# Kernel tuning notes

Hardware: AMD Instinct MI355X
Metric: run time of the kernel (lower is better)

Reference implementation:

```python
import jax, jax.numpy as jnp
import numpy as np

N_USERS = 250000
N_ITEMS = 250000
D = 64          # embedding_dim
H = 64          # hidden_dim
N_EDGES = 1200000
N_NODES = N_USERS + N_ITEMS


def gcn_conv(x, W, b, src, dst, num_nodes):
    """PyG-style GCNConv: add self-loops, symmetric deg normalization, scatter-add."""
    loop = jnp.arange(num_nodes, dtype=src.dtype)
    s = jnp.concatenate([src, loop])
    d = jnp.concatenate([dst, loop])
    deg = jax.ops.segment_sum(jnp.ones(d.shape, x.dtype), d, num_segments=num_nodes)
    dinv = deg ** -0.5  # deg >= 1 thanks to self-loops
    h = x @ W  # [N, H]
    norm = dinv[s] * dinv[d]  # [E']
    msg = h[s] * norm[:, None]  # [E', H] gather
    out = jax.ops.segment_sum(msg, d, num_segments=num_nodes)  # scatter-add
    return out + b


def setup_inputs() -> dict:
    key = jax.random.key(0)
    ks = jax.random.split(key, 8)
    inp = {
        "user_table": jax.random.normal(ks[0], (N_USERS, D), jnp.float32) * 0.1,
        "item_table": jax.random.normal(ks[1], (N_ITEMS, D), jnp.float32) * 0.1,
        "W1": jax.random.normal(ks[2], (D, H), jnp.float32) * (1.0 / np.sqrt(D)),
        "b1": jnp.zeros((H,), jnp.float32),
        "W2": jax.random.normal(ks[3], (H, H), jnp.float32) * (1.0 / np.sqrt(H)),
        "b2": jnp.zeros((H,), jnp.float32),
        "Wp": jax.random.normal(ks[4], (2 * H, 1), jnp.float32) * (1.0 / np.sqrt(2 * H)),
        "bp": jnp.zeros((1,), jnp.float32),
        "edge_index": jax.random.randint(ks[5], (2, N_EDGES), 0, N_NODES, jnp.int32),
        "user_ids": jax.random.randint(ks[6], (N_USERS,), 0, N_USERS, jnp.int32),
        "item_ids": jax.random.randint(ks[7], (N_ITEMS,), 0, N_ITEMS, jnp.int32),
    }
    return inp


def reference(user_table, item_table, W1, b1, W2, b2, Wp, bp,
              edge_index, user_ids, item_ids):
    # embedding bag lookups (one id per bag -> plain gather)
    user_emb = user_table[user_ids]   # [num_users, D]
    item_emb = item_table[item_ids]   # [num_items, D]
    x = jnp.concatenate([user_emb, item_emb], axis=0)  # [N_NODES, D]

    src, dst = edge_index[0], edge_index[1]
    x = jax.nn.relu(gcn_conv(x, W1, b1, src, dst, N_NODES))
    x = jax.nn.relu(gcn_conv(x, W2, b2, src, dst, N_NODES))

    u = x[:N_USERS][user_ids]   # [B, H]
    i = x[N_USERS:][item_ids]   # [B, H]
    combined = jnp.concatenate([u, i], axis=1)  # [B, 2H]
    return combined @ Wp + bp   # [B, 1]
```

## Files before the change

kernel.cpp:

```cpp
#include <hip/hip_runtime.h>

#define NUSERS 250000
#define NITEMS 250000
#define NNODES 500000
#define NEDGES 1200000
#define NGROUPS (NNODES/16)
#define NCH8   (NNODES/8)

#define NB     245
#define BCAP   6144
#define SEGE   8192
#define NBLKA  147

typedef _Float16 half_t;
typedef _Float16 half8 __attribute__((ext_vector_type(8)));
typedef _Float16 half4 __attribute__((ext_vector_type(4)));
typedef float    f32x4 __attribute__((ext_vector_type(4)));


__global__ void k_zero_gc(int* __restrict__ gc) {
    int t = threadIdx.x;
    if (t < NB) gc[t] = 0;
}

__global__ __launch_bounds__(256) void k_bucketA(
    const int* __restrict__ src, const int* __restrict__ dst,
    int* __restrict__ gcursor, unsigned int* __restrict__ gbuf)
{
    __shared__ int ecnt[256];
    __shared__ int ebase[256];
    __shared__ int ecur[256];
    __shared__ int gres[256];
    __shared__ unsigned int stage[SEGE];
    __shared__ unsigned char stb[SEGE];

    const int t = threadIdx.x;
    const int e0 = blockIdx.x * SEGE;
    const int ecount = min(SEGE, NEDGES - e0);

    ecnt[t] = 0;
    __syncthreads();
    for (int k = t; k < ecount; k += 256)
        atomicAdd(&ecnt[dst[e0 + k] >> 11], 1);
    __syncthreads();

    const int v = ecnt[t];
    ebase[t] = v; __syncthreads();
    for (int d = 1; d < 256; d <<= 1) {
        int x = (t >= d) ? ebase[t - d] : 0;
        __syncthreads();
        ebase[t] += x;
        __syncthreads();
    }
    const int excl = ebase[t] - v;
    __syncthreads();
    ebase[t] = excl;
    ecur[t]  = excl;
    if (t < NB && v > 0) gres[t] = atomicAdd(&gcursor[t], v);
    __syncthreads();

    for (int k = t; k < ecount; k += 256) {
        const int s  = src[e0 + k];
        const int d2 = dst[e0 + k];
        const int b  = d2 >> 11;
        const int p  = atomicAdd(&ecur[b], 1);
        stage[p] = ((unsigned int)s << 11) | (unsigned int)(d2 & 2047);
        stb[p]   = (unsigned char)b;
    }
    __syncthreads();

    for (int s = t; s < ecount; s += 256) {
        const int b = stb[s];
        gbuf[(size_t)b * BCAP + gres[b] + (s - ebase[b])] = stage[s];
    }
}

__global__ __launch_bounds__(256) void k_scan_buckets(const int* __restrict__ gcursor,
                                                      int* __restrict__ bbase)
{
    __shared__ int sm[256];
    const int t = threadIdx.x;
    const int v = (t < NB) ? gcursor[t] : 0;
    sm[t] = v; __syncthreads();
    for (int d = 1; d < 256; d <<= 1) {
        int x = (t >= d) ? sm[t - d] : 0;
        __syncthreads();
        sm[t] += x;
        __syncthreads();
    }
    if (t < NB) bbase[t] = sm[t] - v;
}

__global__ __launch_bounds__(256) void k_bucketB(
    const int* __restrict__ gcursor, const int* __restrict__ bbase,
    const unsigned int* __restrict__ gbuf,
    float* __restrict__ dinv, int* __restrict__ offsets, int* __restrict__ csr)
{
    __shared__ int hist[2048];
    __shared__ int cur[2048];
    __shared__ int psum[256];
    __shared__ int lcsr[BCAP];

    const int t = threadIdx.x;
    const int b = blockIdx.x;
    const int cnt = gcursor[b];
    const int nbase = b << 11;
    const int nb = min(2048, NNODES - nbase);
    const unsigned int* gb0 = gbuf + (size_t)b * BCAP;
    const int cbase = bbase[b];

    for (int i = t; i < 2048; i += 256) hist[i] = 0;
    __syncthreads();
    for (int s = t; s < cnt; s += 256)
        atomicAdd(&hist[gb0[s] & 2047], 1);
    __syncthreads();

    for (int i = t; i < nb; i += 256)
        dinv[nbase + i] = 1.0f / sqrtf((float)(hist[i] + 1));

    int loc[8]; int ssum = 0;
#pragma unroll
    for (int k = 0; k < 8; ++k) { loc[k] = hist[t * 8 + k]; ssum += loc[k]; }
    psum[t] = ssum; __syncthreads();
    for (int d = 1; d < 256; d <<= 1) {
        int x = (t >= d) ? psum[t - d] : 0;
        __syncthreads();
        psum[t] += x;
        __syncthreads();
    }
    int run = psum[t] - ssum;
#pragma unroll
    for (int k = 0; k < 8; ++k) {
        const int i = t * 8 + k;
        if (i < nb) offsets[nbase + i] = cbase + run;
        cur[i] = run;
        run += loc[k];
    }
    __syncthreads();
    if (b == NB - 1 && t == 0) offsets[NNODES] = cbase + cnt;

    for (int s = t; s < cnt; s += 256) {
        const unsigned int pk = gb0[s];
        const int p = atomicAdd(&cur[pk & 2047], 1);
        lcsr[p] = (int)(pk >> 11);
    }
    __syncthreads();
    for (int s = t; s < cnt; s += 256)
        csr[cbase + s] = lcsr[s];
}


__device__ __forceinline__ void build_bfrags(const float* __restrict__ W,
                                             int lg, int cl, half8 bf[2][4]) {
#pragma unroll
    for (int q = 0; q < 2; ++q)
#pragma unroll
        for (int c = 0; c < 4; ++c) {
            half8 v;
#pragma unroll
            for (int j = 0; j < 8; ++j)
                v[j] = (half_t)W[(32 * q + 8 * lg + j) * 64 + 4 * cl + c];
            bf[q][c] = v;
        }
}


__global__ __launch_bounds__(256) void k_mm1(
    const float* __restrict__ user_table, const float* __restrict__ item_table,
    const int* __restrict__ uid, const int* __restrict__ iid,
    const float* __restrict__ W1, const float* __restrict__ dinv,
    half_t* __restrict__ g)
{
    const int lane = threadIdx.x & 63;
    const int lg = lane >> 4, cl = lane & 15;
    const int wid = blockIdx.x * (blockDim.x >> 6) + (threadIdx.x >> 6);
    const int nw  = gridDim.x * (blockDim.x >> 6);

    half8 bf[2][4];
    build_bfrags(W1, lg, cl, bf);
    const f32x4 zacc = {0.f, 0.f, 0.f, 0.f};

    if (wid >= NGROUPS) return;

    #define ROWPTR(tt) ({                                                     \
        const int ttc_ = ((tt) < NGROUPS) ? (tt) : wid;                       \
        const int na_ = ttc_ * 16 + cl;                                       \
        (na_ < NUSERS) ? user_table + (size_t)uid[na_] * 64                   \
                       : item_table + (size_t)iid[na_ - NUSERS] * 64; })

    int t = wid;
    const float* pcur  = ROWPTR(t);
    f32x4 u0 = *(const f32x4*)(pcur + 8 * lg);
    f32x4 u1 = *(const f32x4*)(pcur + 8 * lg + 4);
    f32x4 u2 = *(const f32x4*)(pcur + 8 * lg + 32);
    f32x4 u3 = *(const f32x4*)(pcur + 8 * lg + 36);
    const float* pnext = ROWPTR(t + nw);

    while (t < NGROUPS) {
        const int tn = t + nw;
        f32x4 v0 = *(const f32x4*)(pnext + 8 * lg);
        f32x4 v1 = *(const f32x4*)(pnext + 8 * lg + 4);
        f32x4 v2 = *(const f32x4*)(pnext + 8 * lg + 32);
        f32x4 v3 = *(const f32x4*)(pnext + 8 * lg + 36);
        const float* pnn = ROWPTR(tn + nw);

        const int n0 = t * 16;
        half8 a0, a1;
#pragma unroll
        for (int j = 0; j < 4; ++j) {
            a0[j] = (half_t)u0[j]; a0[4 + j] = (half_t)u1[j];
            a1[j] = (half_t)u2[j]; a1[4 + j] = (half_t)u3[j];
        }
        f32x4 acc[4];
#pragma unroll
        for (int c = 0; c < 4; ++c) {
            acc[c] = __builtin_amdgcn_mfma_f32_16x16x32_f16(a0, bf[0][c], zacc, 0, 0, 0);
            acc[c] = __builtin_amdgcn_mfma_f32_16x16x32_f16(a1, bf[1][c], acc[c], 0, 0, 0);
        }
#pragma unroll
        for (int r = 0; r < 4; ++r) {
            const int nd = n0 + lg * 4 + r;
            const float dn = dinv[nd];
            half4 hv;
#pragma unroll
            for (int c = 0; c < 4; ++c) hv[c] = (half_t)(acc[c][r] * dn);
            *(half4*)(g + (size_t)nd * 64 + 4 * cl) = hv;
        }
        u0 = v0; u1 = v1; u2 = v2; u3 = v3;
        pnext = pnn;
        t = tn;
    }
    #undef ROWPTR
}


#define G8_STEP(K)                                                            \
        const bool v##K = sstep + K < deg;                                    \
        const int p##K = csr[v##K ? eb + sstep + K : 0];

#define G8_ROW(K)                                                             \
        const half8 r##K = *(const half8*)(g_p + (size_t)p##K * 64 + sub * 8);

#define G8_ACC(K) {                                                           \
        const float m_ = v##K ? 1.0f : 0.0f;                                  \
        acc0 = fmaf(m_, (float)r##K[0], acc0); acc1 = fmaf(m_, (float)r##K[1], acc1); \
        acc2 = fmaf(m_, (float)r##K[2], acc2); acc3 = fmaf(m_, (float)r##K[3], acc3); \
        acc4 = fmaf(m_, (float)r##K[4], acc4); acc5 = fmaf(m_, (float)r##K[5], acc5); \
        acc6 = fmaf(m_, (float)r##K[6], acc6); acc7 = fmaf(m_, (float)r##K[7], acc7); }

#define GATHER_G8(ginp)                                                       \
    const half_t* __restrict__ g_p = (ginp);                                  \
    const int n  = n0 + gi;                                                   \
    const int eb = off[n];                                                    \
    const int deg = off[n + 1] - eb;                                          \
    float acc0, acc1, acc2, acc3, acc4, acc5, acc6, acc7;                     \
    {                                                                         \
        half8 sv = *(const half8*)(g_p + (size_t)n * 64 + sub * 8);           \
        acc0 = (float)sv[0]; acc1 = (float)sv[1];                             \
        acc2 = (float)sv[2]; acc3 = (float)sv[3];                             \
        acc4 = (float)sv[4]; acc5 = (float)sv[5];                             \
        acc6 = (float)sv[6]; acc7 = (float)sv[7];                             \
    }                                                                         \
    int md = deg;                                                             \
    md = max(md, __shfl_xor(md, 8, 64));                                      \
    md = max(md, __shfl_xor(md, 16, 64));                                     \
    md = max(md, __shfl_xor(md, 32, 64));                                     \
    for (int sstep = 0; sstep < md; sstep += 8) {                             \
        G8_STEP(0) G8_STEP(1) G8_STEP(2) G8_STEP(3)                           \
        G8_STEP(4) G8_STEP(5) G8_STEP(6) G8_STEP(7)                           \
        G8_ROW(0) G8_ROW(1) G8_ROW(2) G8_ROW(3)                               \
        G8_ROW(4) G8_ROW(5) G8_ROW(6) G8_ROW(7)                               \
        G8_ACC(0) G8_ACC(1) G8_ACC(2) G8_ACC(3)                               \
        G8_ACC(4) G8_ACC(5) G8_ACC(6) G8_ACC(7)                               \
    }

__global__ __launch_bounds__(256) void k_gather(
    const int* __restrict__ off, const int* __restrict__ csr,
    const half_t* __restrict__ gin, half_t* __restrict__ sout)
{
    const int lane = threadIdx.x & 63;
    const int gi = lane >> 3;
    const int sub = lane & 7;
    const int wid = blockIdx.x * (blockDim.x >> 6) + (threadIdx.x >> 6);
    const int nw  = gridDim.x * (blockDim.x >> 6);

    for (int t = wid; t < NCH8; t += nw) {
        const int n0 = t * 8;
        GATHER_G8(gin)
        half8 ov;
        ov[0] = (half_t)acc0; ov[1] = (half_t)acc1;
        ov[2] = (half_t)acc2; ov[3] = (half_t)acc3;
        ov[4] = (half_t)acc4; ov[5] = (half_t)acc5;
        ov[6] = (half_t)acc6; ov[7] = (half_t)acc7;
        *(half8*)(sout + (size_t)n * 64 + sub * 8) = ov;
    }
}


__global__ __launch_bounds__(256) void k_mm2(
    const float* __restrict__ W2, const float* __restrict__ b1,
    const float* __restrict__ dinv,
    const half_t* __restrict__ s, half_t* __restrict__ g)
{
    const int lane = threadIdx.x & 63;
    const int lg = lane >> 4, cl = lane & 15;
    const int wid = blockIdx.x * (blockDim.x >> 6) + (threadIdx.x >> 6);
    const int nw  = gridDim.x * (blockDim.x >> 6);

    half8 bf[2][4];
    build_bfrags(W2, lg, cl, bf);
    float bias0[8], bias1[8];
#pragma unroll
    for (int j = 0; j < 8; ++j) {
        bias0[j] = b1[8 * lg + j];
        bias1[j] = b1[32 + 8 * lg + j];
    }
    const f32x4 zacc = {0.f, 0.f, 0.f, 0.f};

    for (int t = wid; t < NGROUPS; t += nw) {
        const int n0 = t * 16;
        const int na = n0 + cl;
        const float dna = dinv[na];
        half8 s0 = *(const half8*)(s + (size_t)na * 64 + 8 * lg);
        half8 s1 = *(const half8*)(s + (size_t)na * 64 + 32 + 8 * lg);
        half8 a0, a1;
#pragma unroll
        for (int j = 0; j < 8; ++j) {
            a0[j] = (half_t)fmaxf(fmaf(dna, (float)s0[j], bias0[j]), 0.0f);
            a1[j] = (half_t)fmaxf(fmaf(dna, (float)s1[j], bias1[j]), 0.0f);
        }
        f32x4 acc[4];
#pragma unroll
        for (int c = 0; c < 4; ++c) {
            acc[c] = __builtin_amdgcn_mfma_f32_16x16x32_f16(a0, bf[0][c], zacc, 0, 0, 0);
            acc[c] = __builtin_amdgcn_mfma_f32_16x16x32_f16(a1, bf[1][c], acc[c], 0, 0, 0);
        }
#pragma unroll
        for (int r = 0; r < 4; ++r) {
            const int nd = n0 + lg * 4 + r;
            const float dn = dinv[nd];
            half4 hv;
#pragma unroll
            for (int c = 0; c < 4; ++c) hv[c] = (half_t)(acc[c][r] * dn);
            *(half4*)(g + (size_t)nd * 64 + 4 * cl) = hv;
        }
    }
}


__global__ __launch_bounds__(256) void k_gather_ps(
    const int* __restrict__ off, const int* __restrict__ csr,
    const float* __restrict__ b2, const float* __restrict__ Wp,
    const float* __restrict__ dinv,
    const half_t* __restrict__ g2, float* __restrict__ pscore)
{
    const int lane = threadIdx.x & 63;
    const int gi = lane >> 3;
    const int sub = lane & 7;
    const int wid = blockIdx.x * (blockDim.x >> 6) + (threadIdx.x >> 6);
    const int nw  = gridDim.x * (blockDim.x >> 6);

    float bb[8], wpu[8], wpi[8];
#pragma unroll
    for (int k = 0; k < 8; ++k) {
        bb[k]  = b2[sub * 8 + k];
        wpu[k] = Wp[sub * 8 + k];
        wpi[k] = Wp[64 + sub * 8 + k];
    }

    for (int t = wid; t < NCH8; t += nw) {
        const int n0 = t * 8;
        GATHER_G8(g2)

        const bool isu = (n0 < NUSERS);
        const float dn = dinv[n];
        float v = 0.0f;
#define PS_ACC(K, A) {                                                      \
        float w_ = isu ? wpu[K] : wpi[K];                                   \
        float x_ = fmaxf(fmaf(dn, (A), bb[K]), 0.0f);                       \
        v = fmaf(x_, w_, v); }
        PS_ACC(0, acc0) PS_ACC(1, acc1) PS_ACC(2, acc2) PS_ACC(3, acc3)
        PS_ACC(4, acc4) PS_ACC(5, acc5) PS_ACC(6, acc6) PS_ACC(7, acc7)
#undef PS_ACC
        v += __shfl_xor(v, 1, 64);
        v += __shfl_xor(v, 2, 64);
        v += __shfl_xor(v, 4, 64);
        if (sub == 0) pscore[n] = v;
    }
}

__global__ void k_pairs(const int* __restrict__ user_ids, const int* __restrict__ item_ids,
                        const float* __restrict__ pscore, const float* __restrict__ bp,
                        float* __restrict__ out)
{
    int b = blockIdx.x * blockDim.x + threadIdx.x;
    if (b < NUSERS)
        out[b] = pscore[user_ids[b]] + pscore[NUSERS + item_ids[b]] + bp[0];
}


extern "C" void kernel_launch(void* const* d_in, const int* in_sizes, int n_in,
                              void* d_out, int out_size, void* d_ws, size_t ws_size,
                              hipStream_t stream)
{
    const float* user_table = (const float*)d_in[0];
    const float* item_table = (const float*)d_in[1];
    const float* W1 = (const float*)d_in[2];
    const float* b1 = (const float*)d_in[3];
    const float* W2 = (const float*)d_in[4];
    const float* b2 = (const float*)d_in[5];
    const float* Wp = (const float*)d_in[6];
    const float* bp = (const float*)d_in[7];
    const int* edge = (const int*)d_in[8];
    const int* uid  = (const int*)d_in[9];
    const int* iid  = (const int*)d_in[10];
    float* out = (float*)d_out;

    const int* src = edge;
    const int* dst = edge + NEDGES;

    char* ws = (char*)d_ws;
    float*        pscore   = (float*)       (ws + 0);
    float*        dinv     = (float*)       (ws + 2000000);
    int*          offsets  = (int*)         (ws + 4000000);
    int*          bbase    = (int*)         (ws + 6000128);
    int*          gcursor  = (int*)         (ws + 6004224);
    int*          csr      = (int*)         (ws + 6008000);
    half_t*       bufA     = (half_t*)      (ws + 10808064);
    half_t*       bufB     = (half_t*)      (ws + 74808064);
    unsigned int* gbuf     = (unsigned int*)(ws + 74808064);

    k_zero_gc     <<<1, 256, 0, stream>>>(gcursor);
    k_bucketA     <<<NBLKA, 256, 0, stream>>>(src, dst, gcursor, gbuf);
    k_scan_buckets<<<1, 256, 0, stream>>>(gcursor, bbase);
    k_bucketB     <<<NB, 256, 0, stream>>>(gcursor, bbase, gbuf, dinv, offsets, csr);

    k_mm1      <<<2048, 256, 0, stream>>>(user_table, item_table, uid, iid, W1, dinv, bufA);
    k_gather   <<<2048, 256, 0, stream>>>(offsets, csr, bufA, bufB);
    k_mm2      <<<2048, 256, 0, stream>>>(W2, b1, dinv, bufB, bufA);
    k_gather_ps<<<2048, 256, 0, stream>>>(offsets, csr, b2, Wp, dinv, bufA, pscore);
    k_pairs    <<<(NUSERS + 255) / 256, 256, 0, stream>>>(uid, iid, pscore, bp, out);
}
```

Before: 201.5 us.

## Fuse layer-1 neighbor gather with second GEMM into one kernel

```diff
diff --git a/kernel.cpp b/kernel.cpp
--- a/kernel.cpp
+++ b/kernel.cpp
@@ -180,29 +180,29 @@
     build_bfrags(W1, lg, cl, bf);
     const f32x4 zacc = {0.f, 0.f, 0.f, 0.f};
 
-    if (wid >= NGROUPS) return;
-
-    #define ROWPTR(tt) ({                                                     \
-        const int ttc_ = ((tt) < NGROUPS) ? (tt) : wid;                       \
-        const int na_ = ttc_ * 16 + cl;                                       \
-        (na_ < NUSERS) ? user_table + (size_t)uid[na_] * 64                   \
-                       : item_table + (size_t)iid[na_ - NUSERS] * 64; })
-
     int t = wid;
-    const float* pcur  = ROWPTR(t);
-    f32x4 u0 = *(const f32x4*)(pcur + 8 * lg);
-    f32x4 u1 = *(const f32x4*)(pcur + 8 * lg + 4);
-    f32x4 u2 = *(const f32x4*)(pcur + 8 * lg + 32);
-    f32x4 u3 = *(const f32x4*)(pcur + 8 * lg + 36);
-    const float* pnext = ROWPTR(t + nw);
-
+    f32x4 u0, u1, u2, u3;
+    if (t < NGROUPS) {
+        const int na = t * 16 + cl;
+        const float* p = (na < NUSERS)
+            ? user_table + (size_t)uid[na] * 64
+            : item_table + (size_t)iid[na - NUSERS] * 64;
+        u0 = *(const f32x4*)(p + 8 * lg);
+        u1 = *(const f32x4*)(p + 8 * lg + 4);
+        u2 = *(const f32x4*)(p + 8 * lg + 32);
+        u3 = *(const f32x4*)(p + 8 * lg + 36);
+    }
     while (t < NGROUPS) {
         const int tn = t + nw;
-        f32x4 v0 = *(const f32x4*)(pnext + 8 * lg);
-        f32x4 v1 = *(const f32x4*)(pnext + 8 * lg + 4);
-        f32x4 v2 = *(const f32x4*)(pnext + 8 * lg + 32);
-        f32x4 v3 = *(const f32x4*)(pnext + 8 * lg + 36);
-        const float* pnn = ROWPTR(tn + nw);
+        const int tl = (tn < NGROUPS) ? tn : t;
+        const int nb2 = tl * 16 + cl;
+        const float* pn = (nb2 < NUSERS)
+            ? user_table + (size_t)uid[nb2] * 64
+            : item_table + (size_t)iid[nb2 - NUSERS] * 64;
+        f32x4 v0 = *(const f32x4*)(pn + 8 * lg);
+        f32x4 v1 = *(const f32x4*)(pn + 8 * lg + 4);
+        f32x4 v2 = *(const f32x4*)(pn + 8 * lg + 32);
+        f32x4 v3 = *(const f32x4*)(pn + 8 * lg + 36);
 
         const int n0 = t * 16;
         half8 a0, a1;
@@ -227,10 +227,116 @@
             *(half4*)(g + (size_t)nd * 64 + 4 * cl) = hv;
         }
         u0 = v0; u1 = v1; u2 = v2; u3 = v3;
-        pnext = pnn;
         t = tn;
     }
-    #undef ROWPTR
+}
+
+
+__global__ __launch_bounds__(256) void k_gather_mm2(
+    const int* __restrict__ off, const int* __restrict__ csr,
+    const float* __restrict__ W2, const float* __restrict__ b1,
+    const float* __restrict__ dinv,
+    const half_t* __restrict__ g1, half_t* __restrict__ g2)
+{
+    const int lane = threadIdx.x & 63;
+    const int lg = lane >> 4, cl = lane & 15;
+    const int wid = blockIdx.x * (blockDim.x >> 6) + (threadIdx.x >> 6);
+    const int nw  = gridDim.x * (blockDim.x >> 6);
+
+    half8 bf[2][4];
+    build_bfrags(W2, lg, cl, bf);
+    float bias0[8], bias1[8];
+#pragma unroll
+    for (int j = 0; j < 8; ++j) {
+        bias0[j] = b1[8 * lg + j];
+        bias1[j] = b1[32 + 8 * lg + j];
+    }
+    const f32x4 zacc = {0.f, 0.f, 0.f, 0.f};
+
+    for (int t = wid; t < NGROUPS; t += nw) {
+        const int n0 = t * 16;
+        const int n  = n0 + cl;
+        const int eb = off[n];
+        const int deg = off[n + 1] - eb;
+
+        float f0[8], f1[8];
+        {
+            half8 s0 = *(const half8*)(g1 + (size_t)n * 64 + 8 * lg);
+            half8 s1 = *(const half8*)(g1 + (size_t)n * 64 + 32 + 8 * lg);
+#pragma unroll
+            for (int j = 0; j < 8; ++j) { f0[j] = (float)s0[j]; f1[j] = (float)s1[j]; }
+        }
+
+        int md = deg;
+        md = max(md, __shfl_xor(md, 1, 64));
+        md = max(md, __shfl_xor(md, 2, 64));
+        md = max(md, __shfl_xor(md, 4, 64));
+        md = max(md, __shfl_xor(md, 8, 64));
+
+        for (int ss = 0; ss < md; ss += 4) {
+            const bool v0 = ss < deg,     v1 = ss + 1 < deg;
+            const bool v2 = ss + 2 < deg, v3 = ss + 3 < deg;
+            const int p0 = csr[v0 ? eb + ss     : 0];
+            const int p1 = csr[v1 ? eb + ss + 1 : 0];
+            const int p2 = csr[v2 ? eb + ss + 2 : 0];
+            const int p3 = csr[v3 ? eb + ss + 3 : 0];
+            const half8 r00 = *(const half8*)(g1 + (size_t)p0 * 64 + 8 * lg);
+            const half8 r01 = *(const half8*)(g1 + (size_t)p0 * 64 + 32 + 8 * lg);
+            const half8 r10 = *(const half8*)(g1 + (size_t)p1 * 64 + 8 * lg);
+            const half8 r11 = *(const half8*)(g1 + (size_t)p1 * 64 + 32 + 8 * lg);
+            const half8 r20 = *(const half8*)(g1 + (size_t)p2 * 64 + 8 * lg);
+            const half8 r21 = *(const half8*)(g1 + (size_t)p2 * 64 + 32 + 8 * lg);
+            const half8 r30 = *(const half8*)(g1 + (size_t)p3 * 64 + 8 * lg);
+            const half8 r31 = *(const half8*)(g1 + (size_t)p3 * 64 + 32 + 8 * lg);
+            const float m0 = v0 ? 1.0f : 0.0f;
+            const float m1 = v1 ? 1.0f : 0.0f;
+            const float m2 = v2 ? 1.0f : 0.0f;
+            const float m3 = v3 ? 1.0f : 0.0f;
+#pragma unroll
+            for (int j = 0; j < 8; ++j) {
+                f0[j] = fmaf(m0, (float)r00[j], f0[j]);
+                f1[j] = fmaf(m0, (float)r01[j], f1[j]);
+            }
+#pragma unroll
+            for (int j = 0; j < 8; ++j) {
+                f0[j] = fmaf(m1, (float)r10[j], f0[j]);
+                f1[j] = fmaf(m1, (float)r11[j], f1[j]);
+            }
+#pragma unroll
+            for (int j = 0; j < 8; ++j) {
+                f0[j] = fmaf(m2, (float)r20[j], f0[j]);
+                f1[j] = fmaf(m2, (float)r21[j], f1[j]);
+            }
+#pragma unroll
+            for (int j = 0; j < 8; ++j) {
+                f0[j] = fmaf(m3, (float)r30[j], f0[j]);
+                f1[j] = fmaf(m3, (float)r31[j], f1[j]);
+            }
+        }
+
+        const float dna = dinv[n];
+        half8 a0, a1;
+#pragma unroll
+        for (int j = 0; j < 8; ++j) {
+            a0[j] = (half_t)fmaxf(fmaf(dna, f0[j], bias0[j]), 0.0f);
+            a1[j] = (half_t)fmaxf(fmaf(dna, f1[j], bias1[j]), 0.0f);
+        }
+        f32x4 acc[4];
+#pragma unroll
+        for (int c = 0; c < 4; ++c) {
+            acc[c] = __builtin_amdgcn_mfma_f32_16x16x32_f16(a0, bf[0][c], zacc, 0, 0, 0);
+            acc[c] = __builtin_amdgcn_mfma_f32_16x16x32_f16(a1, bf[1][c], acc[c], 0, 0, 0);
+        }
+#pragma unroll
+        for (int r = 0; r < 4; ++r) {
+            const int nd = n0 + lg * 4 + r;
+            const float dn = dinv[nd];
+            half4 hv;
+#pragma unroll
+            for (int c = 0; c < 4; ++c) hv[c] = (half_t)(acc[c][r] * dn);
+            *(half4*)(g2 + (size_t)nd * 64 + 4 * cl) = hv;
+        }
+    }
 }
 
 
@@ -274,80 +380,6 @@
         G8_ACC(4) G8_ACC(5) G8_ACC(6) G8_ACC(7)                               \
     }
 
-__global__ __launch_bounds__(256) void k_gather(
-    const int* __restrict__ off, const int* __restrict__ csr,
-    const half_t* __restrict__ gin, half_t* __restrict__ sout)
-{
-    const int lane = threadIdx.x & 63;
-    const int gi = lane >> 3;
-    const int sub = lane & 7;
-    const int wid = blockIdx.x * (blockDim.x >> 6) + (threadIdx.x >> 6);
-    const int nw  = gridDim.x * (blockDim.x >> 6);
-
-    for (int t = wid; t < NCH8; t += nw) {
-        const int n0 = t * 8;
-        GATHER_G8(gin)
-        half8 ov;
-        ov[0] = (half_t)acc0; ov[1] = (half_t)acc1;
-        ov[2] = (half_t)acc2; ov[3] = (half_t)acc3;
-        ov[4] = (half_t)acc4; ov[5] = (half_t)acc5;
-        ov[6] = (half_t)acc6; ov[7] = (half_t)acc7;
-        *(half8*)(sout + (size_t)n * 64 + sub * 8) = ov;
-    }
-}
-
-
-__global__ __launch_bounds__(256) void k_mm2(
-    const float* __restrict__ W2, const float* __restrict__ b1,
-    const float* __restrict__ dinv,
-    const half_t* __restrict__ s, half_t* __restrict__ g)
-{
-    const int lane = threadIdx.x & 63;
-    const int lg = lane >> 4, cl = lane & 15;
-    const int wid = blockIdx.x * (blockDim.x >> 6) + (threadIdx.x >> 6);
-    const int nw  = gridDim.x * (blockDim.x >> 6);
-
-    half8 bf[2][4];
-    build_bfrags(W2, lg, cl, bf);
-    float bias0[8], bias1[8];
-#pragma unroll
-    for (int j = 0; j < 8; ++j) {
-        bias0[j] = b1[8 * lg + j];
-        bias1[j] = b1[32 + 8 * lg + j];
-    }
-    const f32x4 zacc = {0.f, 0.f, 0.f, 0.f};
-
-    for (int t = wid; t < NGROUPS; t += nw) {
-        const int n0 = t * 16;
-        const int na = n0 + cl;
-        const float dna = dinv[na];
-        half8 s0 = *(const half8*)(s + (size_t)na * 64 + 8 * lg);
-        half8 s1 = *(const half8*)(s + (size_t)na * 64 + 32 + 8 * lg);
-        half8 a0, a1;
-#pragma unroll
-        for (int j = 0; j < 8; ++j) {
-            a0[j] = (half_t)fmaxf(fmaf(dna, (float)s0[j], bias0[j]), 0.0f);
-            a1[j] = (half_t)fmaxf(fmaf(dna, (float)s1[j], bias1[j]), 0.0f);
-        }
-        f32x4 acc[4];
-#pragma unroll
-        for (int c = 0; c < 4; ++c) {
-            acc[c] = __builtin_amdgcn_mfma_f32_16x16x32_f16(a0, bf[0][c], zacc, 0, 0, 0);
-            acc[c] = __builtin_amdgcn_mfma_f32_16x16x32_f16(a1, bf[1][c], acc[c], 0, 0, 0);
-        }
-#pragma unroll
-        for (int r = 0; r < 4; ++r) {
-            const int nd = n0 + lg * 4 + r;
-            const float dn = dinv[nd];
-            half4 hv;
-#pragma unroll
-            for (int c = 0; c < 4; ++c) hv[c] = (half_t)(acc[c][r] * dn);
-            *(half4*)(g + (size_t)nd * 64 + 4 * cl) = hv;
-        }
-    }
-}
-
-
 __global__ __launch_bounds__(256) void k_gather_ps(
     const int* __restrict__ off, const int* __restrict__ csr,
     const float* __restrict__ b2, const float* __restrict__ Wp,
@@ -435,9 +467,8 @@
     k_scan_buckets<<<1, 256, 0, stream>>>(gcursor, bbase);
     k_bucketB     <<<NB, 256, 0, stream>>>(gcursor, bbase, gbuf, dinv, offsets, csr);
 
-    k_mm1      <<<2048, 256, 0, stream>>>(user_table, item_table, uid, iid, W1, dinv, bufA);
-    k_gather   <<<2048, 256, 0, stream>>>(offsets, csr, bufA, bufB);
-    k_mm2      <<<2048, 256, 0, stream>>>(W2, b1, dinv, bufB, bufA);
-    k_gather_ps<<<2048, 256, 0, stream>>>(offsets, csr, b2, Wp, dinv, bufA, pscore);
-    k_pairs    <<<(NUSERS + 255) / 256, 256, 0, stream>>>(uid, iid, pscore, bp, out);
-}
+    k_mm1       <<<2048, 256, 0, stream>>>(user_table, item_table, uid, iid, W1, dinv, bufA);
+    k_gather_mm2<<<2048, 256, 0, stream>>>(offsets, csr, W2, b1, dinv, bufA, bufB);
+    k_gather_ps <<<2048, 256, 0, stream>>>(offsets, csr, b2, Wp, dinv, bufB, pscore);
+    k_pairs     <<<(NUSERS + 255) / 256, 256, 0, stream>>>(uid, iid, pscore, bp, out);
+}
```

After: 195.9 us. -2.8%, faster.
